# Kernel optimization log

Hardware: AMD Instinct MI355X
Metric: run time of the kernel (lower is better)

Reference implementation:

```python
import jax, jax.numpy as jnp
import numpy as np

H = 16          # num_heads
D = 64          # head_dim
EPS = 1e-6


def setup_inputs() -> dict:
    key = jax.random.key(0)
    ks = jax.random.split(key, 4)
    B, N, C = 4, 2048, 1024
    x = jax.random.normal(ks[0], (B, N, C), dtype=jnp.float32)
    w_qkv = jax.random.normal(ks[1], (C, 3 * C), dtype=jnp.float32) * (1.0 / np.sqrt(C))
    b_qkv = jnp.zeros((3 * C,), dtype=jnp.float32)
    g_q = jnp.ones((D,), dtype=jnp.float32)
    g_k = jnp.ones((D,), dtype=jnp.float32)
    w_proj = jax.random.normal(ks[2], (C, C), dtype=jnp.float32) * (1.0 / np.sqrt(C))
    b_proj = jnp.zeros((C,), dtype=jnp.float32)
    return {"x": x, "w_qkv": w_qkv, "b_qkv": b_qkv, "g_q": g_q, "g_k": g_k,
            "w_proj": w_proj, "b_proj": b_proj}


def _head_layernorm(t, gamma):
    # LayerNorm over last (head_dim) axis, no bias, with scale. t: [B,H,N,D]
    mu = jnp.mean(t, axis=-1, keepdims=True)
    var = jnp.mean(jnp.square(t - mu), axis=-1, keepdims=True)
    return (t - mu) * jax.lax.rsqrt(var + EPS) * gamma


def reference(x, w_qkv, b_qkv, g_q, g_k, w_proj, b_proj):
    B, N, C = x.shape
    qkv = x @ w_qkv + b_qkv                      # [B, N, 3C]
    qkv = qkv.reshape(B, N, 3, H, D)
    qkv = jnp.transpose(qkv, (2, 0, 3, 1, 4))    # [3, B, H, N, D]
    q, k, v = qkv[0], qkv[1], qkv[2]
    q = _head_layernorm(q, g_q)
    k = _head_layernorm(k, g_k)
    scale = D ** -0.5
    attn = jax.nn.softmax(jnp.einsum('bhqd,bhkd->bhqk', q, k) * scale, axis=-1)
    o = jnp.einsum('bhqk,bhkd->bhqd', attn, v)   # [B, H, N, D]
    o = o.transpose(0, 2, 1, 3).reshape(B, N, C)
    return o @ w_proj + b_proj
```

## Files before the change

kernel.cpp:

```cpp
#include <hip/hip_runtime.h>

#define HH 16
#define DD 64
#define BBATCH 4
#define NSEQ 2048
#define CDIM 1024
#define EPSLN 1e-6f

typedef __bf16 bf16x8 __attribute__((ext_vector_type(8)));
typedef float f32x4 __attribute__((ext_vector_type(4)));
typedef short s16x4 __attribute__((ext_vector_type(4)));
typedef short s16x8 __attribute__((ext_vector_type(8)));
typedef unsigned short u16;

__device__ inline u16 f2b(float f) {
  unsigned u = __builtin_bit_cast(unsigned, f);
  u += 0x7fffu + ((u >> 16) & 1u);
  return (u16)(u >> 16);
}
__device__ inline unsigned pack2(float a, float b) {
  unsigned ua = __builtin_bit_cast(unsigned, a);
  unsigned ub = __builtin_bit_cast(unsigned, b);
  return ((ua + 0x8000u) >> 16) | ((ub + 0x8000u) & 0xffff0000u);
}
#if __has_builtin(__builtin_amdgcn_exp2f)
#define EXP2(x) __builtin_amdgcn_exp2f(x)
#else
#define EXP2(x) __expf((x)*0.6931471805599453f)
#endif

__device__ inline bf16x8 ld_frag16(const u16* p) {
  s16x8 v = *(const s16x8*)p;
  return __builtin_bit_cast(bf16x8, v);
}
__device__ inline f32x4 mfma16(bf16x8 a, bf16x8 b, f32x4 c) {
  return __builtin_amdgcn_mfma_f32_16x16x32_bf16(a, b, c, 0, 0, 0);
}
__device__ inline void async16(const u16* g, u16* l) {
  __builtin_amdgcn_global_load_lds(
      (const __attribute__((address_space(1))) void*)g,
      (__attribute__((address_space(3))) void*)l, 16, 0, 0);
}

__global__ void cvt_x(const float* __restrict__ x, u16* __restrict__ xb) {
  long i = ((long)blockIdx.x * 256 + threadIdx.x) * 8;
  float4 a = *(const float4*)(x + i);
  float4 b = *(const float4*)(x + i + 4);
  u16 r[8];
  r[0] = f2b(a.x); r[1] = f2b(a.y); r[2] = f2b(a.z); r[3] = f2b(a.w);
  r[4] = f2b(b.x); r[5] = f2b(b.y); r[6] = f2b(b.z); r[7] = f2b(b.w);
  *(s16x8*)(xb + i) = *(s16x8*)r;
}

__global__ void cvt_wT(const float* __restrict__ w, u16* __restrict__ wT, int K, int N) {
  __shared__ float tile[32][33];
  int nt = N / 32;
  int bn = blockIdx.x % nt, bk = blockIdx.x / nt;
  int tx = threadIdx.x % 32, ty = threadIdx.x / 32;
  int k0 = bk * 32, n0 = bn * 32;
  for (int j = 0; j < 4; j++)
    tile[ty + 8 * j][tx] = w[(long)(k0 + ty + 8 * j) * N + n0 + tx];
  __syncthreads();
  for (int j = 0; j < 4; j++)
    wT[(long)(n0 + ty + 8 * j) * K + k0 + tx] = f2b(tile[tx][ty + 8 * j]);
}

__launch_bounds__(256, 3)
__global__ void gemm_qkv(const u16* __restrict__ A, const u16* __restrict__ BT,
                         const float* __restrict__ bias,
                         const float* __restrict__ gq, const float* __restrict__ gk,
                         u16* __restrict__ qb, u16* __restrict__ kb, u16* __restrict__ vtb) {
  const int Kd = CDIM;
  __shared__ u16 As[128 * 64];
  __shared__ u16 Bs[128 * 64];
  int t = threadIdx.x;
  int lane = t & 63, wave = t >> 6;
  int ln = lane & 15, quad = lane >> 4;
  int bm = blockIdx.x % 64, bn = blockIdx.x / 64;
  int wm = (wave >> 1) * 64, wn = (wave & 1) * 64;
  int r8 = t >> 3;
  int cb = (t & 7) * 8;
  int cg = (((t & 7) ^ (r8 & 7)) * 8);
  int swl = ln & 7;
  const u16* aB = A + (long)(bm * 128) * Kd + cg;
  const u16* bB = BT + (long)(bn * 128) * Kd + cg;
  f32x4 acc[4][4] = {};
  for (int kt = 0; kt < Kd / 64; kt++) {
    __syncthreads();
#pragma unroll
    for (int c = 0; c < 4; c++) {
      int row = c * 32 + r8;
      async16(aB + (long)row * Kd + kt * 64, As + row * 64 + cb);
      async16(bB + (long)row * Kd + kt * 64, Bs + row * 64 + cb);
    }
    __syncthreads();
#pragma unroll
    for (int kk = 0; kk < 2; kk++) {
      bf16x8 af[4], bfv[4];
#pragma unroll
      for (int mt = 0; mt < 4; mt++)
        af[mt] = ld_frag16(As + (wm + mt * 16 + ln) * 64 + (((kk * 4 + quad) ^ swl) * 8));
#pragma unroll
      for (int nt = 0; nt < 4; nt++)
        bfv[nt] = ld_frag16(Bs + (wn + nt * 16 + ln) * 64 + (((kk * 4 + quad) ^ swl) * 8));
#pragma unroll
      for (int mt = 0; mt < 4; mt++)
#pragma unroll
        for (int nt = 0; nt < 4; nt++)
          acc[mt][nt] = mfma16(af[mt], bfv[nt], acc[mt][nt]);
    }
  }
  int tq = bn >> 3;
  int colbase = bn * 128 + wn;
  int h = (colbase >> 6) & 15;
  int mbase = bm * 128 + wm;
  float bv[4];
#pragma unroll
  for (int nt = 0; nt < 4; nt++) bv[nt] = bias[colbase + nt * 16 + ln];
  if (tq == 2) {
#pragma unroll
    for (int mt = 0; mt < 4; mt++) {
      int m0 = mbase + mt * 16 + quad * 4;
      int b = m0 >> 11, n0 = m0 & 2047;
#pragma unroll
      for (int nt = 0; nt < 4; nt++) {
        int d = nt * 16 + ln;
        u16 pk[4];
#pragma unroll
        for (int r = 0; r < 4; r++) pk[r] = f2b(acc[mt][nt][r] + bv[nt]);
        *(s16x4*)(vtb + ((long)((b * HH + h) * DD + d)) * NSEQ + n0) = *(s16x4*)pk;
      }
    }
  } else {
    const float* g = (tq == 0) ? gq : gk;
    float extra = (tq == 0) ? 0.125f * 1.4426950408889634f : 1.0f;
    u16* dst = (tq == 0) ? qb : kb;
    float gv[4];
#pragma unroll
    for (int nt = 0; nt < 4; nt++) gv[nt] = g[nt * 16 + ln] * extra;
#pragma unroll
    for (int mt = 0; mt < 4; mt++)
#pragma unroll
      for (int r = 0; r < 4; r++) {
        float vv[4];
        float s1 = 0.f, s2 = 0.f;
#pragma unroll
        for (int nt = 0; nt < 4; nt++) {
          vv[nt] = acc[mt][nt][r] + bv[nt];
          s1 += vv[nt];
          s2 += vv[nt] * vv[nt];
        }
#pragma unroll
        for (int m = 1; m < 16; m <<= 1) {
          s1 += __shfl_xor(s1, m);
          s2 += __shfl_xor(s2, m);
        }
        float mu = s1 * (1.0f / 64.0f);
        float var = s2 * (1.0f / 64.0f) - mu * mu;
        float rstd = rsqrtf(var + EPSLN);
        int m = mbase + mt * 16 + quad * 4 + r;
        int b = m >> 11, n = m & 2047;
        long base = ((long)((b * HH + h) * NSEQ + n)) * DD;
#pragma unroll
        for (int nt = 0; nt < 4; nt++)
          dst[base + nt * 16 + ln] = f2b((vv[nt] - mu) * rstd * gv[nt]);
      }
  }
}

__launch_bounds__(256, 2)
__global__ void attn(const u16* __restrict__ qb, const u16* __restrict__ kb,
                     const u16* __restrict__ vtb, u16* __restrict__ ob) {
  __shared__ u16 smem[32768];
  u16* Ks = smem;
  u16* Vs = smem + 8192;
  u16* Pl = smem + 16384;
  int t = threadIdx.x, lane = t & 63, wave = t >> 6;
  int ln = lane & 15, quad = lane >> 4;
  int g = blockIdx.x;
  int bh = (g & 7) * 8 + ((g >> 3) & 7);
  int qblk = g >> 6;
  int b = bh >> 4, h = bh & 15;
  const u16* qg = qb + (long)bh * NSEQ * DD;
  const u16* kg = kb + (long)bh * NSEQ * DD;
  const u16* vg = vtb + (long)bh * DD * NSEQ;
  int qrow0 = qblk * 128 + wave * 32;
  bf16x8 bq[2][2];
#pragma unroll
  for (int qf = 0; qf < 2; qf++)
#pragma unroll
    for (int kk = 0; kk < 2; kk++)
      bq[qf][kk] = ld_frag16(qg + (long)(qrow0 + qf * 16 + ln) * DD + kk * 32 + quad * 8);
  f32x4 o[2][4] = {};
  float rs[2] = {0.f, 0.f};
  u16* Pw0 = Pl + wave * 4096;
  u16* Pw1 = Pw0 + 2048;
  int psw = (ln & 7) * 8;
  int swl = ln & 7;
  int cK = (lane & 7) ^ (lane >> 3);
  int rV = lane >> 4;
  for (int kv = 0; kv < NSEQ / 128; kv++) {
    __syncthreads();
    long kbase = (long)kv * 128 * DD;
#pragma unroll
    for (int c = 0; c < 4; c++) {
      int rowb = c * 32 + wave * 8;
      async16(kg + kbase + (long)(rowb + (lane >> 3)) * 64 + cK * 8,
              Ks + rowb * 64 + lane * 8);
    }
#pragma unroll
    for (int c = 0; c < 4; c++) {
      int drow = c * 16 + wave * 4;
      int rv = drow + rV;
      int cV = (lane & 15) ^ (rv & 7);
      async16(vg + (long)rv * NSEQ + kv * 128 + cV * 8,
              Vs + drow * 128 + lane * 8);
    }
    __syncthreads();
#pragma unroll
    for (int ct = 0; ct < 8; ct++) {
      const u16* ka = Ks + (ct * 16 + ln) * 64;
      bf16x8 k0 = ld_frag16(ka + ((quad ^ swl) * 8));
      bf16x8 k1 = ld_frag16(ka + (((quad + 4) ^ swl) * 8));
      f32x4 z0 = {}, z1 = {};
      z0 = mfma16(k0, bq[0][0], z0);
      z0 = mfma16(k1, bq[0][1], z0);
      z1 = mfma16(k0, bq[1][0], z1);
      z1 = mfma16(k1, bq[1][1], z1);
      int poff = ln * 128 + ((ct * 16 + quad * 4) ^ psw);
      {
        float e0 = EXP2(z0[0]), e1 = EXP2(z0[1]), e2 = EXP2(z0[2]), e3 = EXP2(z0[3]);
        rs[0] += (e0 + e1) + (e2 + e3);
        uint2 pk; pk.x = pack2(e0, e1); pk.y = pack2(e2, e3);
        *(uint2*)(Pw0 + poff) = pk;
      }
      {
        float e0 = EXP2(z1[0]), e1 = EXP2(z1[1]), e2 = EXP2(z1[2]), e3 = EXP2(z1[3]);
        rs[1] += (e0 + e1) + (e2 + e3);
        uint2 pk; pk.x = pack2(e0, e1); pk.y = pack2(e2, e3);
        *(uint2*)(Pw1 + poff) = pk;
      }
    }
    bf16x8 pA[2][4];
#pragma unroll
    for (int kt = 0; kt < 4; kt++) {
      int poff = ln * 128 + ((kt * 32 + quad * 8) ^ psw);
      pA[0][kt] = ld_frag16(Pw0 + poff);
      pA[1][kt] = ld_frag16(Pw1 + poff);
    }
#pragma unroll
    for (int dt = 0; dt < 4; dt++) {
      const u16* vr = Vs + (dt * 16 + ln) * 128;
#pragma unroll
      for (int kt = 0; kt < 4; kt++) {
        bf16x8 vv = ld_frag16(vr + (((4 * kt + quad) ^ swl) * 8));
        o[0][dt] = mfma16(pA[0][kt], vv, o[0][dt]);
        o[1][dt] = mfma16(pA[1][kt], vv, o[1][dt]);
      }
    }
  }
#pragma unroll
  for (int qf = 0; qf < 2; qf++) {
    float r2 = rs[qf];
    r2 += __shfl_xor(r2, 16);
    r2 += __shfl_xor(r2, 32);
#pragma unroll
    for (int r = 0; r < 4; r++) {
      float inv = 1.0f / __shfl(r2, quad * 4 + r);
      int n = qrow0 + qf * 16 + quad * 4 + r;
      long base = ((long)(b * NSEQ + n) * HH + h) * DD;
#pragma unroll
      for (int dt = 0; dt < 4; dt++)
        ob[base + dt * 16 + ln] = f2b(o[qf][dt][r] * inv);
    }
  }
}

__launch_bounds__(256, 3)
__global__ void gemm_proj(const u16* __restrict__ A, const u16* __restrict__ BT,
                          const float* __restrict__ bias, float* __restrict__ out) {
  const int Kd = CDIM;
  __shared__ u16 As[128 * 64];
  __shared__ u16 Bs[128 * 64];
  int t = threadIdx.x;
  int lane = t & 63, wave = t >> 6;
  int ln = lane & 15, quad = lane >> 4;
  int bm = blockIdx.x % 64, bn = blockIdx.x / 64;
  int wm = (wave >> 1) * 64, wn = (wave & 1) * 64;
  int r8 = t >> 3;
  int cb = (t & 7) * 8;
  int cg = (((t & 7) ^ (r8 & 7)) * 8);
  int swl = ln & 7;
  const u16* aB = A + (long)(bm * 128) * Kd + cg;
  const u16* bB = BT + (long)(bn * 128) * Kd + cg;
  f32x4 acc[4][4] = {};
  for (int kt = 0; kt < Kd / 64; kt++) {
    __syncthreads();
#pragma unroll
    for (int c = 0; c < 4; c++) {
      int row = c * 32 + r8;
      async16(aB + (long)row * Kd + kt * 64, As + row * 64 + cb);
      async16(bB + (long)row * Kd + kt * 64, Bs + row * 64 + cb);
    }
    __syncthreads();
#pragma unroll
    for (int kk = 0; kk < 2; kk++) {
      bf16x8 af[4], bfv[4];
#pragma unroll
      for (int mt = 0; mt < 4; mt++)
        af[mt] = ld_frag16(As + (wm + mt * 16 + ln) * 64 + (((kk * 4 + quad) ^ swl) * 8));
#pragma unroll
      for (int nt = 0; nt < 4; nt++)
        bfv[nt] = ld_frag16(Bs + (wn + nt * 16 + ln) * 64 + (((kk * 4 + quad) ^ swl) * 8));
#pragma unroll
      for (int mt = 0; mt < 4; mt++)
#pragma unroll
        for (int nt = 0; nt < 4; nt++)
          acc[mt][nt] = mfma16(af[mt], bfv[nt], acc[mt][nt]);
    }
  }
#pragma unroll
  for (int mt = 0; mt < 4; mt++)
#pragma unroll
    for (int nt = 0; nt < 4; nt++) {
      int col = bn * 128 + wn + nt * 16 + ln;
      float bvx = bias[col];
#pragma unroll
      for (int r = 0; r < 4; r++) {
        int m = bm * 128 + wm + mt * 16 + quad * 4 + r;
        out[(long)m * CDIM + col] = acc[mt][nt][r] + bvx;
      }
    }
}

extern "C" void kernel_launch(void* const* d_in, const int* in_sizes, int n_in,
                              void* d_out, int out_size, void* d_ws, size_t ws_size,
                              hipStream_t stream) {
  const float* x = (const float*)d_in[0];
  const float* w_qkv = (const float*)d_in[1];
  const float* b_qkv = (const float*)d_in[2];
  const float* g_q = (const float*)d_in[3];
  const float* g_k = (const float*)d_in[4];
  const float* w_proj = (const float*)d_in[5];
  const float* b_proj = (const float*)d_in[6];
  float* out = (float*)d_out;

  char* ws = (char*)d_ws;
  const size_t MB = 1024 * 1024;
  u16* xb = (u16*)ws;
  u16* wqkvT = (u16*)(ws + 16 * MB);
  u16* wprojT = (u16*)(ws + 22 * MB);
  u16* qb = (u16*)(ws + 24 * MB);
  u16* kb = (u16*)(ws + 40 * MB);
  u16* vtb = (u16*)(ws + 56 * MB);
  u16* ob = xb;

  cvt_x<<<4096, 256, 0, stream>>>(x, xb);
  cvt_wT<<<(1024 / 32) * (3072 / 32), 256, 0, stream>>>(w_qkv, wqkvT, CDIM, 3 * CDIM);
  cvt_wT<<<(1024 / 32) * (1024 / 32), 256, 0, stream>>>(w_proj, wprojT, CDIM, CDIM);
  gemm_qkv<<<64 * 24, 256, 0, stream>>>(xb, wqkvT, b_qkv, g_q, g_k, qb, kb, vtb);
  attn<<<64 * 16, 256, 0, stream>>>(qb, kb, vtb, ob);
  gemm_proj<<<64 * 8, 256, 0, stream>>>(ob, wprojT, b_proj, out);
}
```

Before: 298.1 us.

## Double attention query tile per block to reuse K/V tiles across more rows

Each attention block now handles 256 query rows (64 per wave) instead of 128, halving the grid to 512 blocks. Each K/V tile staged in LDS is reused across twice as many query rows, cutting global K/V traffic and barrier count per query. To fit the P buffer in LDS, the 128-key chunk is processed in two halves of 64 keys. The bf16 pack also uses a byte-permute builtin. Risks are higher register pressure from the larger accumulator arrays, lower occupancy under launch bounds of 2, and fewer blocks for a 256-CU part.

```diff
diff --git a/kernel.cpp b/kernel.cpp
--- a/kernel.cpp
+++ b/kernel.cpp
@@ -18,11 +18,19 @@
   u += 0x7fffu + ((u >> 16) & 1u);
   return (u16)(u >> 16);
 }
+#if __has_builtin(__builtin_amdgcn_perm)
+__device__ inline unsigned pack2(float a, float b) {
+  unsigned ua = __builtin_bit_cast(unsigned, a) + 0x8000u;
+  unsigned ub = __builtin_bit_cast(unsigned, b) + 0x8000u;
+  return __builtin_amdgcn_perm(ub, ua, 0x07060302u);
+}
+#else
 __device__ inline unsigned pack2(float a, float b) {
   unsigned ua = __builtin_bit_cast(unsigned, a);
   unsigned ub = __builtin_bit_cast(unsigned, b);
   return ((ua + 0x8000u) >> 16) | ((ub + 0x8000u) & 0xffff0000u);
 }
+#endif
 #if __has_builtin(__builtin_amdgcn_exp2f)
 #define EXP2(x) __builtin_amdgcn_exp2f(x)
 #else
@@ -179,22 +187,21 @@
   int ln = lane & 15, quad = lane >> 4;
   int g = blockIdx.x;
   int bh = (g & 7) * 8 + ((g >> 3) & 7);
-  int qblk = g >> 6;
+  int qblk = (g >> 6) & 7;
   int b = bh >> 4, h = bh & 15;
   const u16* qg = qb + (long)bh * NSEQ * DD;
   const u16* kg = kb + (long)bh * NSEQ * DD;
   const u16* vg = vtb + (long)bh * DD * NSEQ;
-  int qrow0 = qblk * 128 + wave * 32;
-  bf16x8 bq[2][2];
-#pragma unroll
-  for (int qf = 0; qf < 2; qf++)
+  int qrow0 = qblk * 256 + wave * 64;
+  bf16x8 bq[4][2];
+#pragma unroll
+  for (int qf = 0; qf < 4; qf++)
 #pragma unroll
     for (int kk = 0; kk < 2; kk++)
       bq[qf][kk] = ld_frag16(qg + (long)(qrow0 + qf * 16 + ln) * DD + kk * 32 + quad * 8);
-  f32x4 o[2][4] = {};
-  float rs[2] = {0.f, 0.f};
-  u16* Pw0 = Pl + wave * 4096;
-  u16* Pw1 = Pw0 + 2048;
+  f32x4 o[4][4] = {};
+  float rs[4] = {0.f, 0.f, 0.f, 0.f};
+  u16* Pw = Pl + wave * 4096;
   int psw = (ln & 7) * 8;
   int swl = ln & 7;
   int cK = (lane & 7) ^ (lane >> 3);
@@ -218,49 +225,49 @@
     }
     __syncthreads();
 #pragma unroll
-    for (int ct = 0; ct < 8; ct++) {
-      const u16* ka = Ks + (ct * 16 + ln) * 64;
-      bf16x8 k0 = ld_frag16(ka + ((quad ^ swl) * 8));
-      bf16x8 k1 = ld_frag16(ka + (((quad + 4) ^ swl) * 8));
-      f32x4 z0 = {}, z1 = {};
-      z0 = mfma16(k0, bq[0][0], z0);
-      z0 = mfma16(k1, bq[0][1], z0);
-      z1 = mfma16(k0, bq[1][0], z1);
-      z1 = mfma16(k1, bq[1][1], z1);
-      int poff = ln * 128 + ((ct * 16 + quad * 4) ^ psw);
-      {
-        float e0 = EXP2(z0[0]), e1 = EXP2(z0[1]), e2 = EXP2(z0[2]), e3 = EXP2(z0[3]);
-        rs[0] += (e0 + e1) + (e2 + e3);
-        uint2 pk; pk.x = pack2(e0, e1); pk.y = pack2(e2, e3);
-        *(uint2*)(Pw0 + poff) = pk;
-      }
-      {
-        float e0 = EXP2(z1[0]), e1 = EXP2(z1[1]), e2 = EXP2(z1[2]), e3 = EXP2(z1[3]);
-        rs[1] += (e0 + e1) + (e2 + e3);
-        uint2 pk; pk.x = pack2(e0, e1); pk.y = pack2(e2, e3);
-        *(uint2*)(Pw1 + poff) = pk;
-      }
-    }
-    bf16x8 pA[2][4];
-#pragma unroll
-    for (int kt = 0; kt < 4; kt++) {
-      int poff = ln * 128 + ((kt * 32 + quad * 8) ^ psw);
-      pA[0][kt] = ld_frag16(Pw0 + poff);
-      pA[1][kt] = ld_frag16(Pw1 + poff);
-    }
-#pragma unroll
-    for (int dt = 0; dt < 4; dt++) {
-      const u16* vr = Vs + (dt * 16 + ln) * 128;
-#pragma unroll
-      for (int kt = 0; kt < 4; kt++) {
-        bf16x8 vv = ld_frag16(vr + (((4 * kt + quad) ^ swl) * 8));
-        o[0][dt] = mfma16(pA[0][kt], vv, o[0][dt]);
-        o[1][dt] = mfma16(pA[1][kt], vv, o[1][dt]);
-      }
-    }
-  }
-#pragma unroll
-  for (int qf = 0; qf < 2; qf++) {
+    for (int half = 0; half < 2; half++) {
+#pragma unroll
+      for (int ctl = 0; ctl < 4; ctl++) {
+        int ct = half * 4 + ctl;
+        const u16* ka = Ks + (ct * 16 + ln) * 64;
+        bf16x8 k0 = ld_frag16(ka + ((quad ^ swl) * 8));
+        bf16x8 k1 = ld_frag16(ka + (((quad + 4) ^ swl) * 8));
+        int poffc = (ctl * 16 + quad * 4) ^ psw;
+#pragma unroll
+        for (int qf = 0; qf < 4; qf++) {
+          f32x4 z = {};
+          z = mfma16(k0, bq[qf][0], z);
+          z = mfma16(k1, bq[qf][1], z);
+          float e0 = EXP2(z[0]), e1 = EXP2(z[1]), e2 = EXP2(z[2]), e3 = EXP2(z[3]);
+          rs[qf] += (e0 + e1) + (e2 + e3);
+          uint2 pk;
+          pk.x = pack2(e0, e1);
+          pk.y = pack2(e2, e3);
+          *(uint2*)(Pw + (qf * 16 + ln) * 64 + poffc) = pk;
+        }
+      }
+      bf16x8 pA[4][2];
+#pragma unroll
+      for (int qf = 0; qf < 4; qf++)
+#pragma unroll
+        for (int ktl = 0; ktl < 2; ktl++)
+          pA[qf][ktl] = ld_frag16(Pw + (qf * 16 + ln) * 64 + ((ktl * 32 + quad * 8) ^ psw));
+#pragma unroll
+      for (int dt = 0; dt < 4; dt++) {
+        const u16* vr = Vs + (dt * 16 + ln) * 128;
+#pragma unroll
+        for (int ktl = 0; ktl < 2; ktl++) {
+          int kt = half * 2 + ktl;
+          bf16x8 vv = ld_frag16(vr + (((4 * kt + quad) ^ swl) * 8));
+#pragma unroll
+          for (int qf = 0; qf < 4; qf++)
+            o[qf][dt] = mfma16(pA[qf][ktl], vv, o[qf][dt]);
+        }
+      }
+    }
+  }
+#pragma unroll
+  for (int qf = 0; qf < 4; qf++) {
     float r2 = rs[qf];
     r2 += __shfl_xor(r2, 16);
     r2 += __shfl_xor(r2, 32);
@@ -359,6 +366,6 @@
   cvt_wT<<<(1024 / 32) * (3072 / 32), 256, 0, stream>>>(w_qkv, wqkvT, CDIM, 3 * CDIM);
   cvt_wT<<<(1024 / 32) * (1024 / 32), 256, 0, stream>>>(w_proj, wprojT, CDIM, CDIM);
   gemm_qkv<<<64 * 24, 256, 0, stream>>>(xb, wqkvT, b_qkv, g_q, g_k, qb, kb, vtb);
-  attn<<<64 * 16, 256, 0, stream>>>(qb, kb, vtb, ob);
+  attn<<<512, 256, 0, stream>>>(qb, kb, vtb, ob);
   gemm_proj<<<64 * 8, 256, 0, stream>>>(ob, wprojT, b_proj, out);
 }
```

Measured after the change: 272.5 us. 8.6% less time.
